# Kernel tuning notes

Measured on AMD Instinct MI355X. Metric: run time of the kernel, lower is better.

Reference implementation:

```python
import jax, jax.numpy as jnp
import numpy as np

NUM_HEADS = 16
LN_EPS = 1e-5
ROPE_BASE = 10000.0


def _rope_tables(frames, head_dim, dtype):
    inv_freq = 1.0 / (ROPE_BASE ** (jnp.arange(0, head_dim, 2, dtype=jnp.float32) / head_dim))
    pos = jnp.arange(frames, dtype=jnp.float32)
    freqs = jnp.outer(pos, inv_freq)            # [T, hd/2]
    freqs = jnp.concatenate([freqs, freqs], -1)  # [T, hd]
    return jnp.cos(freqs).astype(dtype), jnp.sin(freqs).astype(dtype)


def _apply_rope(x, cos, sin):
    # x: [..., T, hd]; cos/sin broadcast over leading dims
    half = x.shape[-1] // 2
    x1, x2 = x[..., :half], x[..., half:]
    rotated = jnp.concatenate([-x2, x1], -1)
    return x * cos + rotated * sin


def setup_inputs() -> dict:
    key = jax.random.key(0)
    k1, k2, k3 = jax.random.split(key, 3)
    hidden = 1024
    B, frames, height, width = 2, 16, 32, 32
    seq_len = frames * height * width
    x = jax.random.normal(k1, (B, seq_len, hidden), dtype=jnp.float32)
    w_qkv = jax.random.normal(k2, (3 * hidden, hidden), dtype=jnp.float32) * (hidden ** -0.5)
    w_out = jax.random.normal(k3, (hidden, hidden), dtype=jnp.float32) * (hidden ** -0.5)
    return {
        "x": x,
        "w_qkv": w_qkv,
        "w_out": w_out,
        "ln_gamma": jnp.ones((hidden,), jnp.float32),
        "ln_beta": jnp.zeros((hidden,), jnp.float32),
        "height": height,
        "width": width,
        "frames": frames,
    }


def reference(x, w_qkv, w_out, ln_gamma, ln_beta, height, width, frames):
    B, seq_len, hidden = x.shape
    spatial = height * width
    nh = NUM_HEADS
    hd = hidden // nh
    scale = hd ** -0.5

    # LayerNorm
    mu = jnp.mean(x, -1, keepdims=True)
    var = jnp.var(x, -1, keepdims=True)
    xn = (x - mu) * jax.lax.rsqrt(var + LN_EPS) * ln_gamma + ln_beta

    # [B, T, S, D] -> [B*S, T, D]
    xt = xn.reshape(B, frames, spatial, hidden).transpose(0, 2, 1, 3)
    xt = xt.reshape(B * spatial, frames, hidden)

    qkv = jnp.einsum('ntd,ed->nte', xt, w_qkv)  # [N, T, 3*hidden]
    qkv = qkv.reshape(B * spatial, frames, 3, nh, hd)
    q, k, v = qkv[:, :, 0], qkv[:, :, 1], qkv[:, :, 2]  # [N, T, nh, hd]
    q = q.transpose(0, 2, 1, 3)  # [N, nh, T, hd]
    k = k.transpose(0, 2, 1, 3)
    v = v.transpose(0, 2, 1, 3)

    cos, sin = _rope_tables(frames, hd, x.dtype)  # [T, hd]
    q = _apply_rope(q, cos, sin)
    k = _apply_rope(k, cos, sin)

    attn = jnp.einsum('nhqd,nhkd->nhqk', q, k) * scale
    causal_mask = jnp.triu(jnp.ones((frames, frames), jnp.bool_), k=1)
    attn = jnp.where(causal_mask, -jnp.inf, attn)
    attn = jax.nn.softmax(attn.astype(jnp.float32), axis=-1).astype(x.dtype)

    out = jnp.einsum('nhqk,nhkd->nhqd', attn, v)  # [N, nh, T, hd]
    out = out.transpose(0, 2, 1, 3).reshape(B, spatial, frames, hidden)
    out = out.transpose(0, 2, 1, 3).reshape(B, seq_len, hidden)
    return jnp.einsum('bsd,ed->bse', out, w_out)
```

## Files before the change

### kernel.cpp

```cpp
#include <hip/hip_runtime.h>
#include <stdint.h>

typedef __attribute__((ext_vector_type(4))) uint16_t u16x4;
typedef __attribute__((ext_vector_type(8))) uint16_t u16x8;
typedef __attribute__((ext_vector_type(8))) __bf16  bf16x8;
typedef __attribute__((ext_vector_type(4))) float   f32x4;

__device__ __forceinline__ uint16_t f2bf(float f) {
  uint32_t x = __float_as_uint(f);
  x += 0x7fffu + ((x >> 16) & 1u);
  return (uint16_t)(x >> 16);
}
__device__ __forceinline__ f32x4 mfma32(bf16x8 a, bf16x8 b, f32x4 c) {
  return __builtin_amdgcn_mfma_f32_16x16x32_bf16(a, b, c, 0, 0, 0);
}
__device__ __forceinline__ void gld16(const uint16_t* g, uint16_t* s) {
  __builtin_amdgcn_global_load_lds(
      (const __attribute__((address_space(1))) void*)g,
      (__attribute__((address_space(3))) void*)s, 16, 0, 0);
}


__global__ __launch_bounds__(256)
void conv_w(const float* __restrict__ wq, const float* __restrict__ wo,
            uint16_t* __restrict__ dst) {
  int i = blockIdx.x * 256 + threadIdx.x;
  float4 v = (i < 786432) ? ((const float4*)wq)[i]
                          : ((const float4*)wo)[i - 786432];
  u16x4 o;
  o[0] = f2bf(v.x); o[1] = f2bf(v.y); o[2] = f2bf(v.z); o[3] = f2bf(v.w);
  ((u16x4*)dst)[i] = o;
}

__global__ __launch_bounds__(256)
void ln_chunk(const float* __restrict__ x, const float* __restrict__ gw,
              const float* __restrict__ bw, uint16_t* __restrict__ xt, int c0) {
  const int wv = threadIdx.x >> 6, lane = threadIdx.x & 63;
  const int r = blockIdx.x * 4 + wv;
  const int nl = r >> 4, t = r & 15;
  const int n = c0 + nl, b = n >> 10, sp = n & 1023;
  const float* xr = x + ((size_t)b * 16384 + (size_t)t * 1024 + sp) * 1024;
  float4 v[4];
#pragma unroll
  for (int c = 0; c < 4; ++c) v[c] = ((const float4*)xr)[c * 64 + lane];
  float s = 0.f, ss = 0.f;
#pragma unroll
  for (int c = 0; c < 4; ++c) {
    s  += v[c].x + v[c].y + v[c].z + v[c].w;
    ss += v[c].x * v[c].x + v[c].y * v[c].y + v[c].z * v[c].z + v[c].w * v[c].w;
  }
#pragma unroll
  for (int o = 32; o > 0; o >>= 1) { s += __shfl_xor(s, o); ss += __shfl_xor(ss, o); }
  const float mu = s * (1.f / 1024.f);
  const float var = ss * (1.f / 1024.f) - mu * mu;
  const float rs = rsqrtf(var + 1e-5f);
  uint16_t* orow = xt + (size_t)r * 1024;
#pragma unroll
  for (int c = 0; c < 4; ++c) {
    float4 g = ((const float4*)gw)[c * 64 + lane];
    float4 be = ((const float4*)bw)[c * 64 + lane];
    u16x4 o;
    o[0] = f2bf((v[c].x - mu) * rs * g.x + be.x);
    o[1] = f2bf((v[c].y - mu) * rs * g.y + be.y);
    o[2] = f2bf((v[c].z - mu) * rs * g.z + be.z);
    o[3] = f2bf((v[c].w - mu) * rs * g.w + be.w);
    ((u16x4*)orow)[c * 64 + lane] = o;
  }
}

template <int EPI>
__global__ __launch_bounds__(512)
void gemm_bt(const uint16_t* __restrict__ A, const uint16_t* __restrict__ B,
             uint16_t* __restrict__ C0, uint16_t* __restrict__ C1,
             uint16_t* __restrict__ C2, float* __restrict__ F0, int c0, int lgc) {
  __shared__ __align__(16) uint16_t As[2][16384];
  __shared__ __align__(16) uint16_t Bs[2][16384];
  const int tid = threadIdx.x, lane = tid & 63, w = tid >> 6;
  const int bn = blockIdx.x, bm = blockIdx.y;
  const int srow = lane >> 3;
  const int schunk = (lane & 7) ^ srow;
  const uint16_t* ga = A + (size_t)(bm * 256 + w * 32 + srow) * 1024 + schunk * 8;
  const uint16_t* gb = B + (size_t)(bn * 256 + w * 32 + srow) * 1024 + schunk * 8;
  const int sOff = w * 2048;
  const int wm = w >> 2, wn = w & 3;
  const int fr = lane & 15, quad = lane >> 4;
  f32x4 acc[8][4];
#pragma unroll
  for (int i = 0; i < 8; ++i)
#pragma unroll
    for (int j = 0; j < 4; ++j) acc[i][j] = (f32x4){0.f, 0.f, 0.f, 0.f};

  auto compute = [&](int cur) {
#pragma unroll
    for (int ko = 0; ko < 2; ++ko) {
      const int kchunk = ((ko * 4 + quad) ^ (fr & 7)) * 8;
      bf16x8 a[8], b[4];
#pragma unroll
      for (int tm = 0; tm < 8; ++tm)
        a[tm] = *(const bf16x8*)&As[cur][(wm * 128 + tm * 16 + fr) * 64 + kchunk];
#pragma unroll
      for (int tn = 0; tn < 4; ++tn)
        b[tn] = *(const bf16x8*)&Bs[cur][(wn * 64 + tn * 16 + fr) * 64 + kchunk];
#pragma unroll
      for (int tm = 0; tm < 8; ++tm)
#pragma unroll
        for (int tn = 0; tn < 4; ++tn)
          acc[tm][tn] = mfma32(a[tm], b[tn], acc[tm][tn]);
    }
  };

#pragma unroll
  for (int i = 0; i < 4; ++i) {
    gld16(ga + (size_t)i * 8192, &As[0][sOff + i * 512]);
    gld16(gb + (size_t)i * 8192, &Bs[0][sOff + i * 512]);
  }
  ga += 64; gb += 64;

  for (int kt = 0; kt < 15; ++kt) {
    const int cur = kt & 1;
#pragma unroll
    for (int i = 0; i < 4; ++i) {
      gld16(ga + (size_t)i * 8192, &As[cur ^ 1][sOff + i * 512]);
      gld16(gb + (size_t)i * 8192, &Bs[cur ^ 1][sOff + i * 512]);
    }
    ga += 64; gb += 64;
    __builtin_amdgcn_sched_barrier(0);
    asm volatile("s_waitcnt vmcnt(8)" ::: "memory");
    __builtin_amdgcn_sched_barrier(0);
    __builtin_amdgcn_s_barrier();
    __builtin_amdgcn_sched_barrier(0);
    compute(cur);
    __builtin_amdgcn_sched_barrier(0);
    __builtin_amdgcn_s_barrier();
  }
  __builtin_amdgcn_sched_barrier(0);
  asm volatile("s_waitcnt vmcnt(0)" ::: "memory");
  __builtin_amdgcn_sched_barrier(0);
  __builtin_amdgcn_s_barrier();
  __builtin_amdgcn_sched_barrier(0);
  compute(1);

  if (EPI == 0) {
#pragma unroll
    for (int tm = 0; tm < 8; ++tm) {
#pragma unroll
      for (int tn = 0; tn < 4; ++tn) {
        int colg = bn * 256 + wn * 64 + tn * 16 + fr;
#pragma unroll
        for (int r = 0; r < 4; ++r) {
          int l = bm * 256 + wm * 128 + tm * 16 + quad * 4 + r;
          int t = l >> lgc, nl = l & ((1 << lgc) - 1);
          int n = c0 + nl, b = n >> 10, sp = n & 1023;
          size_t grow = (size_t)b * 16384 + (size_t)t * 1024 + sp;
          F0[grow * 1024 + colg] = acc[tm][tn][r];
        }
      }
    }
  } else {
    float* cosT = (float*)As;
    float* sinT = (float*)&Bs[0][0];
    __syncthreads();
    for (int idx = tid; idx < 512; idx += 512) {
      int t = idx >> 5, i = idx & 31;
      float ang = (float)t * expf(-(float)i * 0.28782313662425574f);
      cosT[idx] = cosf(ang);
      sinT[idx] = sinf(ang);
    }
    __syncthreads();
    const int e0 = bn * 256 + wn * 64;
    const int which = e0 >> 10;
    const int h = (e0 >> 6) & 15;
    const int n_base = bm * 16 + wm * 8;
    if (which == 2) {
#pragma unroll
      for (int tm = 0; tm < 8; ++tm) {
        size_t base = ((size_t)(n_base + tm) * 16 + h) * 1024 + (size_t)(quad * 4) * 64;
#pragma unroll
        for (int tn = 0; tn < 4; ++tn) {
          int d = tn * 16 + fr;
#pragma unroll
          for (int r = 0; r < 4; ++r)
            C2[base + (size_t)r * 64 + d] = f2bf(acc[tm][tn][r]);
        }
      }
    } else {
      uint16_t* dst = (which == 0) ? C0 : C1;
      const float sc = (which == 0) ? 0.125f : 1.0f;
#pragma unroll
      for (int tm = 0; tm < 8; ++tm) {
        size_t base0 = ((size_t)(n_base + tm) * 16 + h) * 1024;
#pragma unroll
        for (int tn2 = 0; tn2 < 2; ++tn2) {
          int d1 = tn2 * 16 + fr;
#pragma unroll
          for (int r = 0; r < 4; ++r) {
            int t = quad * 4 + r;
            float c = cosT[t * 32 + d1], s = sinT[t * 32 + d1];
            float x1 = acc[tm][tn2][r], x2 = acc[tm][tn2 + 2][r];
            dst[base0 + (size_t)t * 64 + d1]      = f2bf((x1 * c - x2 * s) * sc);
            dst[base0 + (size_t)t * 64 + d1 + 32] = f2bf((x2 * c + x1 * s) * sc);
          }
        }
      }
    }
  }
}

__global__ __launch_bounds__(256)
void attn_chunk(const uint16_t* __restrict__ q, const uint16_t* __restrict__ k,
                const uint16_t* __restrict__ v, uint16_t* __restrict__ out,
                int chunkN) {
  __shared__ float sPT[4][16][17];
  const int wv = threadIdx.x >> 6, lane = threadIdx.x & 63;
  const int pair = blockIdx.x * 4 + wv;
  const int nl = pair >> 4, h = pair & 15;
  const uint16_t* qb = q + (size_t)pair * 1024;
  const uint16_t* kb = k + (size_t)pair * 1024;
  const uint16_t* vb = v + (size_t)pair * 1024;
  const int col = lane & 15, quad = lane >> 4;
  const int ro = col * 64 + quad * 8;
  bf16x8 ka0 = *(const bf16x8*)(kb + ro);
  bf16x8 ka1 = *(const bf16x8*)(kb + ro + 32);
  bf16x8 qa0 = *(const bf16x8*)(qb + ro);
  bf16x8 qa1 = *(const bf16x8*)(qb + ro + 32);
  f32x4 s4 = (f32x4){0.f, 0.f, 0.f, 0.f};
  s4 = mfma32(ka0, qa0, s4);
  s4 = mfma32(ka1, qa1, s4);
  float p[4];
  float mx = -3.0e38f;
#pragma unroll
  for (int r = 0; r < 4; ++r) {
    int tk = quad * 4 + r;
    p[r] = (tk <= col) ? s4[r] : -3.0e38f;
    mx = fmaxf(mx, p[r]);
  }
  mx = fmaxf(mx, __shfl_xor(mx, 16));
  mx = fmaxf(mx, __shfl_xor(mx, 32));
  float sum = 0.f;
#pragma unroll
  for (int r = 0; r < 4; ++r) {
    p[r] = (p[r] <= -1.0e38f) ? 0.f : expf(p[r] - mx);
    sum += p[r];
  }
  sum += __shfl_xor(sum, 16);
  sum += __shfl_xor(sum, 32);
  const float inv = 1.f / sum;
#pragma unroll
  for (int r = 0; r < 4; ++r) sPT[wv][quad * 4 + r][col] = p[r] * inv;
  __syncthreads();
  bf16x8 pa;
#pragma unroll
  for (int j = 0; j < 8; ++j) {
    float pv = (quad < 2) ? sPT[wv][(quad * 8 + j) & 15][col] : 0.f;
    pa[j] = (__bf16)pv;
  }
  const __bf16* vbf = (const __bf16*)vb;
#pragma unroll
  for (int dt = 0; dt < 4; ++dt) {
    bf16x8 bv;
#pragma unroll
    for (int j = 0; j < 8; ++j) {
      int tk = (quad * 8 + j) & 15;
      __bf16 val = vbf[tk * 64 + dt * 16 + col];
      bv[j] = (quad < 2) ? val : (__bf16)0.f;
    }
    f32x4 o = (f32x4){0.f, 0.f, 0.f, 0.f};
    o = mfma32(pa, bv, o);
#pragma unroll
    for (int r = 0; r < 4; ++r) {
      int t = quad * 4 + r;
      out[((size_t)t * chunkN + nl) * 1024 + h * 64 + dt * 16 + col] = f2bf(o[r]);
    }
  }
}

extern "C" void kernel_launch(void* const* d_in, const int* in_sizes, int n_in,
                              void* d_out, int out_size, void* d_ws, size_t ws_size,
                              hipStream_t stream) {
  const float* x     = (const float*)d_in[0];
  const float* w_qkv = (const float*)d_in[1];
  const float* w_out = (const float*)d_in[2];
  const float* gamma = (const float*)d_in[3];
  const float* beta  = (const float*)d_in[4];
  float* out = (float*)d_out;

  uint16_t* wqb = (uint16_t*)d_ws;
  uint16_t* wob = wqb + 3145728;
  uint16_t* base = wob + 1048576;
  const size_t wbytes = 4194304ull * 2;
  size_t avail = (ws_size > wbytes) ? ws_size - wbytes : 0;
  size_t chunkN = 2048;
  while (chunkN > 16 && chunkN * 131072ull > avail) chunkN >>= 1;
  int lgc = 31 - __builtin_clz((unsigned)chunkN);
  const int nch = (int)(2048 / chunkN);
  const size_t seg = chunkN * 16384;
  uint16_t* xt = base;
  uint16_t* qb = xt + seg;
  uint16_t* kb = qb + seg;
  uint16_t* vb = kb + seg;

  conv_w<<<dim3(4096), dim3(256), 0, stream>>>(w_qkv, w_out, wqb);
  for (int c = 0; c < nch; ++c) {
    const int c0 = c * (int)chunkN;
    ln_chunk<<<dim3((uint32_t)chunkN * 4), dim3(256), 0, stream>>>(
        x, gamma, beta, xt, c0);
    gemm_bt<1><<<dim3(12, (uint32_t)chunkN / 16), dim3(512), 0, stream>>>(
        xt, wqb, qb, kb, vb, nullptr, 0, 0);
    attn_chunk<<<dim3((uint32_t)chunkN * 4), dim3(256), 0, stream>>>(
        qb, kb, vb, xt, (int)chunkN);
    gemm_bt<0><<<dim3(4, (uint32_t)chunkN / 16), dim3(512), 0, stream>>>(
        xt, wob, nullptr, nullptr, nullptr, out, c0, lgc);
  }
}
```

Before: 627.8 us.

## Interleave GEMM prefetch with MFMA phases using barriers and setprio

Restructures the bf16 GEMM main loop so each K-tile is split into four sub-phases (two k-halves by two M-halves), issuing the next tile's global-to-LDS loads after the first LDS reads and wrapping the MFMA groups in s_setprio and workgroup barriers. This aims at a ping-pong style schedule where waves overlap LDS reads, global loads and matrix math instead of waiting on memory at a single point per tile. It adds more barriers per iteration and waits for all loads at the end of each tile, which could serialize more if the overlap does not materialize. The RoPE table loop is also rewritten as a simple guarded block, which has no speed effect.

```diff
diff --git a/kernel.cpp b/kernel.cpp
--- a/kernel.cpp
+++ b/kernel.cpp
@@ -19,6 +19,7 @@
       (const __attribute__((address_space(1))) void*)g,
       (__attribute__((address_space(3))) void*)s, 16, 0, 0);
 }
+#define SB0() __builtin_amdgcn_sched_barrier(0)
 
 
 __global__ __launch_bounds__(256)
@@ -90,55 +91,63 @@
 #pragma unroll
     for (int j = 0; j < 4; ++j) acc[i][j] = (f32x4){0.f, 0.f, 0.f, 0.f};
 
-  auto compute = [&](int cur) {
-#pragma unroll
-    for (int ko = 0; ko < 2; ++ko) {
-      const int kchunk = ((ko * 4 + quad) ^ (fr & 7)) * 8;
-      bf16x8 a[8], b[4];
-#pragma unroll
-      for (int tm = 0; tm < 8; ++tm)
-        a[tm] = *(const bf16x8*)&As[cur][(wm * 128 + tm * 16 + fr) * 64 + kchunk];
-#pragma unroll
-      for (int tn = 0; tn < 4; ++tn)
-        b[tn] = *(const bf16x8*)&Bs[cur][(wn * 64 + tn * 16 + fr) * 64 + kchunk];
-#pragma unroll
-      for (int tm = 0; tm < 8; ++tm)
-#pragma unroll
-        for (int tn = 0; tn < 4; ++tn)
-          acc[tm][tn] = mfma32(a[tm], b[tn], acc[tm][tn]);
-    }
-  };
-
 #pragma unroll
   for (int i = 0; i < 4; ++i) {
     gld16(ga + (size_t)i * 8192, &As[0][sOff + i * 512]);
     gld16(gb + (size_t)i * 8192, &Bs[0][sOff + i * 512]);
   }
   ga += 64; gb += 64;
-
-  for (int kt = 0; kt < 15; ++kt) {
+  SB0();
+  asm volatile("s_waitcnt vmcnt(0)" ::: "memory");
+  SB0();
+  __builtin_amdgcn_s_barrier();
+  SB0();
+
+  for (int kt = 0; kt < 16; ++kt) {
     const int cur = kt & 1;
-#pragma unroll
-    for (int i = 0; i < 4; ++i) {
-      gld16(ga + (size_t)i * 8192, &As[cur ^ 1][sOff + i * 512]);
-      gld16(gb + (size_t)i * 8192, &Bs[cur ^ 1][sOff + i * 512]);
-    }
-    ga += 64; gb += 64;
-    __builtin_amdgcn_sched_barrier(0);
-    asm volatile("s_waitcnt vmcnt(8)" ::: "memory");
-    __builtin_amdgcn_sched_barrier(0);
-    __builtin_amdgcn_s_barrier();
-    __builtin_amdgcn_sched_barrier(0);
-    compute(cur);
-    __builtin_amdgcn_sched_barrier(0);
-    __builtin_amdgcn_s_barrier();
-  }
-  __builtin_amdgcn_sched_barrier(0);
-  asm volatile("s_waitcnt vmcnt(0)" ::: "memory");
-  __builtin_amdgcn_sched_barrier(0);
-  __builtin_amdgcn_s_barrier();
-  __builtin_amdgcn_sched_barrier(0);
-  compute(1);
+    const uint16_t* as = As[cur];
+    const uint16_t* bs = Bs[cur];
+#pragma unroll
+    for (int ko = 0; ko < 2; ++ko) {
+      const int kchunk = ((ko * 4 + quad) ^ (fr & 7)) * 8;
+      bf16x8 b[4];
+#pragma unroll
+      for (int tn = 0; tn < 4; ++tn)
+        b[tn] = *(const bf16x8*)&bs[(wn * 64 + tn * 16 + fr) * 64 + kchunk];
+#pragma unroll
+      for (int h = 0; h < 2; ++h) {
+        bf16x8 a[4];
+#pragma unroll
+        for (int t = 0; t < 4; ++t)
+          a[t] = *(const bf16x8*)&as[(wm * 128 + (h * 4 + t) * 16 + fr) * 64 + kchunk];
+        if (ko == 0 && h == 0 && kt < 15) {
+#pragma unroll
+          for (int i = 0; i < 4; ++i) {
+            gld16(ga + (size_t)i * 8192, &As[cur ^ 1][sOff + i * 512]);
+            gld16(gb + (size_t)i * 8192, &Bs[cur ^ 1][sOff + i * 512]);
+          }
+          ga += 64; gb += 64;
+        }
+        SB0();
+        __builtin_amdgcn_s_barrier();
+        SB0();
+        __builtin_amdgcn_s_setprio(1);
+#pragma unroll
+        for (int t = 0; t < 4; ++t)
+#pragma unroll
+          for (int tn = 0; tn < 4; ++tn)
+            acc[h * 4 + t][tn] = mfma32(a[t], b[tn], acc[h * 4 + t][tn]);
+        __builtin_amdgcn_s_setprio(0);
+        SB0();
+        if (ko == 1 && h == 1) {
+          asm volatile("s_waitcnt vmcnt(0)" ::: "memory");
+          SB0();
+        }
+        __builtin_amdgcn_s_barrier();
+        SB0();
+      }
+    }
+  }
 
   if (EPI == 0) {
 #pragma unroll
@@ -160,11 +169,11 @@
     float* cosT = (float*)As;
     float* sinT = (float*)&Bs[0][0];
     __syncthreads();
-    for (int idx = tid; idx < 512; idx += 512) {
-      int t = idx >> 5, i = idx & 31;
+    if (tid < 512) {
+      int t = tid >> 5, i = tid & 31;
       float ang = (float)t * expf(-(float)i * 0.28782313662425574f);
-      cosT[idx] = cosf(ang);
-      sinT[idx] = sinf(ang);
+      cosT[tid] = cosf(ang);
+      sinT[tid] = sinf(ang);
     }
     __syncthreads();
     const int e0 = bn * 256 + wn * 64;
```

New measurement: 638.2 us. Within noise of the previous version (+1.7%).
